# Optimization experiments

Hardware: AMD Instinct MI355X
Metric: run time of the kernel (lower is better)

Reference implementation:

```python
import jax, jax.numpy as jnp
import numpy as np

D_MODEL, D_K, D_V, H, N, B = 512, 64, 64, 8, 2048, 2


def _xavier(key, shape):
    fan_out, fan_in = shape
    a = jnp.sqrt(6.0 / (fan_in + fan_out))
    return jax.random.uniform(key, shape, jnp.float32, -a, a)


def setup_inputs() -> dict:
    key = jax.random.key(0)
    ks = jax.random.split(key, 12)
    inp = {
        "regions_out": jax.random.normal(ks[0], (B, N, D_MODEL), jnp.float32),
        "grids_out": jax.random.normal(ks[1], (B, N, D_MODEL), jnp.float32),
        "interests": jax.random.normal(ks[2], (B, N, D_MODEL), jnp.float32),
        "attention_mask_regions": jax.random.randint(ks[3], (B, 1, 1, N), 0, 2, jnp.int32),
        "attention_mask_grids": jax.random.randint(ks[4], (B, 1, 1, N), 0, 2, jnp.int32),
        "attention_weights": jax.random.uniform(ks[5], (B, 1, 1, N), jnp.float32),
        # nn.Linear params (weight [out,in], bias [out]); xavier_uniform weights, zero bias
        "Wq": _xavier(ks[6], (H * D_K, D_MODEL)), "bq": jnp.zeros((H * D_K,), jnp.float32),
        "Wk": _xavier(ks[7], (H * D_K, D_MODEL)), "bk": jnp.zeros((H * D_K,), jnp.float32),
        "Wv": _xavier(ks[8], (H * D_V, D_MODEL)), "bv": jnp.zeros((H * D_V,), jnp.float32),
        "Wq12": _xavier(ks[9], (H * D_K, D_MODEL)), "bq12": jnp.zeros((H * D_K,), jnp.float32),
        "Wo1": _xavier(ks[10], (D_MODEL, H * D_V)), "bo1": jnp.zeros((D_MODEL,), jnp.float32),
        "Wo2": _xavier(ks[11], (D_MODEL, H * D_V)), "bo2": jnp.zeros((D_MODEL,), jnp.float32),
    }
    return inp


def _proj(x, W, b, d):
    # x: [b, n, d_model] -> [b, h, n, d]
    b_s, n, _ = x.shape
    y = x @ W.T + b
    return y.reshape(b_s, n, H, d).transpose(0, 2, 1, 3)


def reference(regions_out, grids_out, interests, attention_mask_regions,
              attention_mask_grids, attention_weights,
              Wq, bq, Wk, bk, Wv, bv, Wq12, bq12, Wo1, bo1, Wo2, bo2):
    b_s, nq, _ = interests.shape
    scale = 1.0 / np.sqrt(D_K).astype(np.float32)

    q = _proj(interests, Wq, bq, D_K)          # [b,h,nq,dk]
    q1 = _proj(regions_out, Wq12, bq12, D_K)   # [b,h,nk1,dk]
    q2 = _proj(grids_out, Wq12, bq12, D_K)     # [b,h,nk1,dk]
    k1 = _proj(regions_out, Wk, bk, D_K)       # [b,h,nk1,dk]
    k2 = _proj(grids_out, Wk, bk, D_K)
    v1 = _proj(regions_out, Wv, bv, D_V)
    v2 = _proj(grids_out, Wv, bv, D_V)

    att1 = jnp.einsum("bhqd,bhkd->bhqk", q + q2, k1) * scale
    att2 = jnp.einsum("bhqd,bhkd->bhqk", q + q1, k2) * scale
    att1 = att1 * attention_weights
    att2 = att2 * attention_weights
    att1 = jnp.where(attention_mask_regions.astype(bool), -jnp.inf, att1)
    att2 = jnp.where(attention_mask_grids.astype(bool), -jnp.inf, att2)
    att1 = jax.nn.softmax(att1, axis=-1)
    att2 = jax.nn.softmax(att2, axis=-1)
    # dropout is identity in eval mode

    out1 = jnp.einsum("bhqk,bhkd->bhqd", att1, v1).transpose(0, 2, 1, 3).reshape(b_s, nq, H * D_V)
    out2 = jnp.einsum("bhqk,bhkd->bhqd", att2, v2).transpose(0, 2, 1, 3).reshape(b_s, nq, H * D_V)
    out1 = out1 @ Wo1.T + bo1
    out2 = out2 @ Wo2.T + bo2
    return (out1, out2)
```

## Files before the change

kernel.cpp:

```cpp
#include <hip/hip_runtime.h>
#include <hip/hip_bf16.h>

typedef __attribute__((ext_vector_type(8))) __bf16 bf16x8;
typedef __attribute__((ext_vector_type(4))) float f32x4;
typedef __attribute__((ext_vector_type(4))) int   i32x4;
typedef unsigned short u16;

#define WS_SEG 2097152

static __device__ __forceinline__ u16 f2b(float f) {
  __hip_bfloat16 h = __float2bfloat16(f);
  return __builtin_bit_cast(u16, h);
}
static __device__ __forceinline__ i32x4 cvt8(const float* __restrict__ p) {
  float4 a = *(const float4*)p;
  float4 b = *(const float4*)(p + 4);
  union { i32x4 v; u16 u[8]; } r;
  r.u[0]=f2b(a.x); r.u[1]=f2b(a.y); r.u[2]=f2b(a.z); r.u[3]=f2b(a.w);
  r.u[4]=f2b(b.x); r.u[5]=f2b(b.y); r.u[6]=f2b(b.z); r.u[7]=f2b(b.w);
  return r.v;
}
static __device__ __forceinline__ float fexp2(float x) {
  float r; asm("v_exp_f32 %0, %1" : "=v"(r) : "v"(x)); return r;
}
template<int C>
static __device__ __forceinline__ float dppf(float x) {
  int v = __builtin_amdgcn_update_dpp(__builtin_bit_cast(int, x),
                                      __builtin_bit_cast(int, x), C, 0xF, 0xF, false);
  return __builtin_bit_cast(float, v);
}
static __device__ __forceinline__ float rowsum16(float x) {
  x += dppf<0xB1>(x);
  x += dppf<0x4E>(x);
  x += dppf<0x141>(x);
  x += dppf<0x140>(x);
  return x;
}
static __device__ __forceinline__ void gld16(const u16* gp, u16* lp) {
  __builtin_amdgcn_global_load_lds(
      (const __attribute__((address_space(1))) void*)gp,
      (__attribute__((address_space(3))) void*)lp, 16, 0, 0);
}

__global__ __launch_bounds__(256) void convert_kernel(
    const float* __restrict__ regions, const float* __restrict__ grids,
    const float* __restrict__ interests,
    const float* __restrict__ Wq, const float* __restrict__ Wk,
    const float* __restrict__ Wv, const float* __restrict__ Wq12,
    const float* __restrict__ Wo1, const float* __restrict__ Wo2,
    u16* __restrict__ ws)
{
  const size_t i = (size_t)(blockIdx.x * 256 + threadIdx.x) * 8;
  const float* s; u16* d;
  if (i < 2097152)      { s = regions   + i;           d = ws + 6 * WS_SEG + i; }
  else if (i < 4194304) { s = grids     + (i - 2097152); d = ws + 7 * WS_SEG + (i - 2097152); }
  else if (i < 6291456) { s = interests + (i - 4194304); d = ws + 8 * WS_SEG + (i - 4194304); }
  else {
    const size_t j = i - 6291456;
    d = ws + 9 * WS_SEG + j;
    if (j < 262144)       s = Wq  + j;
    else if (j < 524288)  s = Wk  + (j - 262144);
    else if (j < 786432)  s = Wv  + (j - 524288);
    else if (j < 1048576) s = Wq12+ (j - 786432);
    else if (j < 1310720) s = Wo1 + (j - 1048576);
    else                  s = Wo2 + (j - 1310720);
  }
  *(i32x4*)d = cvt8(s);
}

template<int MT>
__global__ __launch_bounds__(256, 2) void gemm_all(
    const float* __restrict__ aw,
    const float* __restrict__ bq,  const float* __restrict__ bk,
    const float* __restrict__ bv,  const float* __restrict__ bq12,
    const float* __restrict__ bo1, const float* __restrict__ bo2,
    u16* __restrict__ ws, float* __restrict__ out, int phase)
{
  __shared__ u16 As[MT * 64];
  __shared__ u16 Bs[128 * 64];
  constexpr int MFR = MT / 32;

  const u16* regs_bf = ws + 6 * WS_SEG;
  const u16* grid_bf = ws + 7 * WS_SEG;
  const u16* intr_bf = ws + 8 * WS_SEG;
  const u16* Wt      = ws + 9 * WS_SEG;

  const u16 *A1 = nullptr, *A2 = nullptr, *B1 = nullptr, *B2 = nullptr;
  const float *bias1 = nullptr, *bias2 = nullptr;
  u16* dst16 = nullptr;
  float* dst32 = nullptr;
  int KT = 512, epi = 0;
  const int z = blockIdx.z;
  if (phase == 0) {
    if (z == 0)      { A1=intr_bf; A2=grid_bf; B1=Wt; B2=Wt+786432; KT=1024; bias1=bq; bias2=bq12; epi=0; dst16=ws+0*WS_SEG; }
    else if (z == 1) { A1=intr_bf; A2=regs_bf; B1=Wt; B2=Wt+786432; KT=1024; bias1=bq; bias2=bq12; epi=0; dst16=ws+1*WS_SEG; }
    else if (z == 2) { A1=regs_bf; B1=Wt+262144; bias1=bk; epi=1; dst16=ws+2*WS_SEG; }
    else if (z == 3) { A1=grid_bf; B1=Wt+262144; bias1=bk; epi=1; dst16=ws+3*WS_SEG; }
    else if (z == 4) { A1=regs_bf; B1=Wt+524288; bias1=bv; epi=3; dst16=ws+4*WS_SEG; }
    else             { A1=grid_bf; B1=Wt+524288; bias1=bv; epi=3; dst16=ws+5*WS_SEG; }
  } else {
    if (z == 0) { A1=ws+6*WS_SEG; B1=Wt+1048576; bias1=bo1; epi=2; dst32=out; }
    else        { A1=ws+7*WS_SEG; B1=Wt+1310720; bias1=bo2; epi=2; dst32=out + 2097152; }
  }
  const bool swp = (epi == 3);

  const int t = threadIdx.x;
  const int lane = t & 63, w = t >> 6;
  const int l15 = lane & 15, q4 = lane >> 4;
  const int m0 = blockIdx.y * MT, j0 = blockIdx.x * 128;
  const int ro = (w >> 1) * (MT / 2), co = (w & 1) * 64;

  f32x4 acc[MFR][4];
  for (int i = 0; i < MFR; i++)
    for (int j = 0; j < 4; j++) acc[i][j] = (f32x4){0.f, 0.f, 0.f, 0.f};

  for (int k0 = 0; k0 < KT; k0 += 64) {
    const u16* pa; const u16* pb; int kk = k0, ra, rb;
    if (swp)           { pa = B1; pb = A1; ra = j0; rb = m0; }
    else if (kk < 512) { pa = A1; pb = B1; ra = m0; rb = j0; }
    else               { pa = A2; pb = B2; ra = m0; rb = j0; kk -= 512; }
    __syncthreads();
#pragma unroll
    for (int c = 0; c < MFR; c++) {
      const int cidx = w * MFR + c;
      const int row = cidx * 8 + (lane >> 3);
      const int cg = (lane & 7) ^ (row & 7);
      gld16(&pa[(ra + row) * 512 + kk + cg * 8], &As[cidx * 512]);
    }
#pragma unroll
    for (int c = 0; c < 4; c++) {
      const int cidx = w * 4 + c;
      const int row = cidx * 8 + (lane >> 3);
      const int cg = (lane & 7) ^ (row & 7);
      gld16(&pb[(rb + row) * 512 + kk + cg * 8], &Bs[cidx * 512]);
    }
    __syncthreads();
#pragma unroll
    for (int h = 0; h < 2; h++) {
      bf16x8 af[MFR], bfr[4];
#pragma unroll
      for (int i = 0; i < MFR; i++) {
        const int r = ro + i * 16 + l15;
        af[i] = *(const bf16x8*)&As[r * 64 + (((h * 4 + q4) ^ (r & 7)) * 8)];
      }
#pragma unroll
      for (int i = 0; i < 4; i++) {
        const int r = co + i * 16 + l15;
        bfr[i] = *(const bf16x8*)&Bs[r * 64 + (((h * 4 + q4) ^ (r & 7)) * 8)];
      }
#pragma unroll
      for (int mt = 0; mt < MFR; mt++)
#pragma unroll
        for (int nt = 0; nt < 4; nt++)
          acc[mt][nt] = __builtin_amdgcn_mfma_f32_16x16x32_bf16(af[mt], bfr[nt], acc[mt][nt], 0, 0, 0);
    }
  }

#pragma unroll
  for (int nt = 0; nt < 4; nt++) {
    if (epi == 3) {
      const int token = m0 + co + nt * 16 + l15;
      const int bb = token >> 11, nn = token & 2047;
#pragma unroll
      for (int mt = 0; mt < MFR; mt++)
#pragma unroll
        for (int r = 0; r < 4; r++) {
          const int hd = j0 + ro + mt * 16 + q4 * 4 + r;
          dst16[(bb * 512 + hd) * 2048 + nn] = f2b(acc[mt][nt][r] + bias1[hd]);
        }
    } else {
      const int j = j0 + co + nt * 16 + l15;
      float bsum = bias1[j];
      if (bias2) bsum += bias2[j];
#pragma unroll
      for (int mt = 0; mt < MFR; mt++)
#pragma unroll
        for (int r = 0; r < 4; r++) {
          const int m = m0 + ro + mt * 16 + q4 * 4 + r;
          float v = acc[mt][nt][r] + bsum;
          if (epi == 2) {
            dst32[m * 512 + j] = v;
          } else {
            const int b = m >> 11, nn = m & 2047, h = j >> 6, d = j & 63;
            if (epi == 1) v *= 0.18033688f * aw[b * 2048 + nn];
            dst16[((b * 8 + h) * 2048 + nn) * 64 + d] = f2b(v);
          }
        }
    }
  }
}

__global__ __launch_bounds__(256, 2) void attn_kernel(
    const int* __restrict__ mask_r, const int* __restrict__ mask_g,
    u16* __restrict__ ws)
{
  const int qt = blockIdx.x, bh = blockIdx.y, path = blockIdx.z;
  const int b = bh >> 3, h = bh & 7;
  const u16* Q  = (path ? ws + 1 * WS_SEG : ws + 0 * WS_SEG) + bh * (2048 * 64);
  const u16* K  = (path ? ws + 3 * WS_SEG : ws + 2 * WS_SEG) + bh * (2048 * 64);
  const u16* Vg = (path ? ws + 5 * WS_SEG : ws + 4 * WS_SEG) + (b * 512 + h * 64) * 2048;
  const int* mask = (path ? mask_g : mask_r) + b * 2048;
  u16* O = (path ? ws + 7 * WS_SEG : ws + 6 * WS_SEG) + (b * 2048 + qt * 128) * 512 + h * 64;

  __shared__ u16 Ks[64 * 64];
  __shared__ u16 Vs[64 * 64];
  __shared__ u16 Ps[128 * 64];
  __shared__ float Ms[2048];

  const int t = threadIdx.x, lane = t & 63, w = t >> 6;
  const int l15 = lane & 15, q4 = lane >> 4;

  {
    const int4 a = *(const int4*)&mask[t * 8];
    const int4 c = *(const int4*)&mask[t * 8 + 4];
    float4 f1, f2v;
    f1.x = (a.x ? -1e30f : 0.f) - 16.f; f1.y = (a.y ? -1e30f : 0.f) - 16.f;
    f1.z = (a.z ? -1e30f : 0.f) - 16.f; f1.w = (a.w ? -1e30f : 0.f) - 16.f;
    f2v.x = (c.x ? -1e30f : 0.f) - 16.f; f2v.y = (c.y ? -1e30f : 0.f) - 16.f;
    f2v.z = (c.z ? -1e30f : 0.f) - 16.f; f2v.w = (c.w ? -1e30f : 0.f) - 16.f;
    *(float4*)&Ms[t * 8] = f1;
    *(float4*)&Ms[t * 8 + 4] = f2v;
  }

  bf16x8 qf[2][2];
#pragma unroll
  for (int mt = 0; mt < 2; mt++) {
    const int qrow = qt * 128 + w * 32 + mt * 16 + l15;
    qf[mt][0] = *(const bf16x8*)&Q[qrow * 64 + q4 * 8];
    qf[mt][1] = *(const bf16x8*)&Q[qrow * 64 + 32 + q4 * 8];
  }

  float l_run[2][4];
  f32x4 o_acc[2][4];
#pragma unroll
  for (int mt = 0; mt < 2; mt++) {
#pragma unroll
    for (int r = 0; r < 4; r++) l_run[mt][r] = 0.f;
#pragma unroll
    for (int d = 0; d < 4; d++) o_acc[mt][d] = (f32x4){0.f, 0.f, 0.f, 0.f};
  }

  for (int kt = 0; kt < 32; kt++) {
    __syncthreads();
#pragma unroll
    for (int c = 0; c < 2; c++) {
      const int cidx = w * 2 + c;
      const int row = cidx * 8 + (lane >> 3);
      const int cg = (lane & 7) ^ (row & 7);
      gld16(&K[(kt * 64 + row) * 64 + cg * 8], &Ks[cidx * 512]);
      gld16(&Vg[row * 2048 + kt * 64 + cg * 8], &Vs[cidx * 512]);
    }
    __syncthreads();

    f32x4 s[2][4];
#pragma unroll
    for (int mt = 0; mt < 2; mt++)
#pragma unroll
      for (int nt = 0; nt < 4; nt++) s[mt][nt] = (f32x4){0.f, 0.f, 0.f, 0.f};
#pragma unroll
    for (int nt = 0; nt < 4; nt++)
#pragma unroll
      for (int ss = 0; ss < 2; ss++) {
        const int r = nt * 16 + l15;
        bf16x8 kf = *(const bf16x8*)&Ks[r * 64 + (((ss * 4 + q4) ^ (r & 7)) * 8)];
        s[0][nt] = __builtin_amdgcn_mfma_f32_16x16x32_bf16(qf[0][ss], kf, s[0][nt], 0, 0, 0);
        s[1][nt] = __builtin_amdgcn_mfma_f32_16x16x32_bf16(qf[1][ss], kf, s[1][nt], 0, 0, 0);
      }

#pragma unroll
    for (int nt = 0; nt < 4; nt++) {
      const float bias = Ms[kt * 64 + nt * 16 + l15];
#pragma unroll
      for (int mt = 0; mt < 2; mt++)
#pragma unroll
        for (int r = 0; r < 4; r++) {
          const float p = fexp2(s[mt][nt][r] + bias);
          s[mt][nt][r] = p;
          l_run[mt][r] += p;
        }
    }

#pragma unroll
    for (int mt = 0; mt < 2; mt++)
#pragma unroll
      for (int nt = 0; nt < 4; nt++) {
        const int cg = 2 * nt + (l15 >> 3);
#pragma unroll
        for (int r = 0; r < 4; r++) {
          const int row = w * 32 + mt * 16 + q4 * 4 + r;
          Ps[row * 64 + ((cg ^ (row & 7)) * 8) + (l15 & 7)] = f2b(s[mt][nt][r]);
        }
      }
    asm volatile("s_waitcnt lgkmcnt(0)" ::: "memory");

#pragma unroll
    for (int ss = 0; ss < 2; ss++) {
      bf16x8 pf[2];
#pragma unroll
      for (int mt = 0; mt < 2; mt++) {
        const int row = w * 32 + mt * 16 + l15;
        const int cg = (4 * ss + q4) ^ (row & 7);
        pf[mt] = *(const bf16x8*)&Ps[row * 64 + cg * 8];
      }
#pragma unroll
      for (int dt = 0; dt < 4; dt++) {
        const int r = dt * 16 + l15;
        bf16x8 vf = *(const bf16x8*)&Vs[r * 64 + (((ss * 4 + q4) ^ (r & 7)) * 8)];
        o_acc[0][dt] = __builtin_amdgcn_mfma_f32_16x16x32_bf16(pf[0], vf, o_acc[0][dt], 0, 0, 0);
        o_acc[1][dt] = __builtin_amdgcn_mfma_f32_16x16x32_bf16(pf[1], vf, o_acc[1][dt], 0, 0, 0);
      }
    }
  }

#pragma unroll
  for (int mt = 0; mt < 2; mt++)
#pragma unroll
    for (int r = 0; r < 4; r++) {
      const float inv = 1.f / rowsum16(l_run[mt][r]);
#pragma unroll
      for (int dt = 0; dt < 4; dt++) {
        O[(w * 32 + mt * 16 + q4 * 4 + r) * 512 + dt * 16 + l15] = f2b(o_acc[mt][dt][r] * inv);
      }
    }
}

extern "C" void kernel_launch(void* const* d_in, const int* in_sizes, int n_in,
                              void* d_out, int out_size, void* d_ws, size_t ws_size,
                              hipStream_t stream) {
  const float* regions   = (const float*)d_in[0];
  const float* grids     = (const float*)d_in[1];
  const float* interests = (const float*)d_in[2];
  const int*   mask_r    = (const int*)d_in[3];
  const int*   mask_g    = (const int*)d_in[4];
  const float* aw        = (const float*)d_in[5];
  const float* Wq  = (const float*)d_in[6];  const float* bq  = (const float*)d_in[7];
  const float* Wk  = (const float*)d_in[8];  const float* bk  = (const float*)d_in[9];
  const float* Wv  = (const float*)d_in[10]; const float* bv  = (const float*)d_in[11];
  const float* Wq12= (const float*)d_in[12]; const float* bq12= (const float*)d_in[13];
  const float* Wo1 = (const float*)d_in[14]; const float* bo1 = (const float*)d_in[15];
  const float* Wo2 = (const float*)d_in[16]; const float* bo2 = (const float*)d_in[17];
  u16*   ws  = (u16*)d_ws;
  float* out = (float*)d_out;

  convert_kernel<<<3840, 256, 0, stream>>>(regions, grids, interests,
      Wq, Wk, Wv, Wq12, Wo1, Wo2, ws);
  gemm_all<128><<<dim3(4, 32, 6), 256, 0, stream>>>(aw, bq, bk, bv, bq12, bo1, bo2,
      ws, out, 0);
  attn_kernel<<<dim3(16, 16, 2), 256, 0, stream>>>(mask_r, mask_g, ws);
  gemm_all<64><<<dim3(4, 64, 2), 256, 0, stream>>>(aw, bq, bk, bv, bq12, bo1, bo2,
      ws, out, 1);
}
```

Baseline: 202.4 us.

## Stage GEMM and attention epilogues through LDS for coalesced 16-byte stores

The projection GEMM epilogue now writes bf16 results into swizzled shared memory and then issues coalesced 16-byte global stores instead of scattered 2-byte stores. The Q/K layout changes from head-major [b,h,n,64] to token-major [b,n,512], and the attention kernel's addressing is updated to match. The attention output is staged through Ps the same way before being stored. This aims to cut uncoalesced store traffic, at the cost of extra LDS round trips and syncs that rely on the per-wave LDS regions not overlapping.

Result: no change. 203.7 us (+0.6%).

```diff
diff --git a/kernel.cpp b/kernel.cpp
--- a/kernel.cpp
+++ b/kernel.cpp
@@ -156,36 +156,69 @@
     }
   }
 
-#pragma unroll
-  for (int nt = 0; nt < 4; nt++) {
-    if (epi == 3) {
-      const int token = m0 + co + nt * 16 + l15;
-      const int bb = token >> 11, nn = token & 2047;
-#pragma unroll
-      for (int mt = 0; mt < MFR; mt++)
-#pragma unroll
-        for (int r = 0; r < 4; r++) {
-          const int hd = j0 + ro + mt * 16 + q4 * 4 + r;
-          dst16[(bb * 512 + hd) * 2048 + nn] = f2b(acc[mt][nt][r] + bias1[hd]);
-        }
-    } else {
+  if (epi == 2) {
+#pragma unroll
+    for (int nt = 0; nt < 4; nt++) {
       const int j = j0 + co + nt * 16 + l15;
-      float bsum = bias1[j];
-      if (bias2) bsum += bias2[j];
+      const float bsum = bias1[j];
 #pragma unroll
       for (int mt = 0; mt < MFR; mt++)
 #pragma unroll
         for (int r = 0; r < 4; r++) {
           const int m = m0 + ro + mt * 16 + q4 * 4 + r;
-          float v = acc[mt][nt][r] + bsum;
-          if (epi == 2) {
-            dst32[m * 512 + j] = v;
-          } else {
-            const int b = m >> 11, nn = m & 2047, h = j >> 6, d = j & 63;
-            if (epi == 1) v *= 0.18033688f * aw[b * 2048 + nn];
-            dst16[((b * 8 + h) * 2048 + nn) * 64 + d] = f2b(v);
-          }
+          dst32[m * 512 + j] = acc[mt][nt][r] + bsum;
         }
+    }
+    return;
+  }
+
+  __syncthreads();
+  u16* Es = ((w < 2) ? As : Bs) + (w & 1) * 4096;
+
+  if (epi == 3) {
+#pragma unroll
+    for (int mt = 0; mt < MFR; mt++)
+#pragma unroll
+      for (int r = 0; r < 4; r++) {
+        const int rr = mt * 16 + q4 * 4 + r;
+        const float bias = bias1[j0 + ro + rr];
+#pragma unroll
+        for (int nt = 0; nt < 4; nt++)
+          Es[rr * 64 + (((nt * 2 + (l15 >> 3)) ^ (rr & 7)) * 8) + (l15 & 7)] =
+              f2b(acc[mt][nt][r] + bias);
+      }
+  } else {
+    float bsum4[4];
+#pragma unroll
+    for (int nt = 0; nt < 4; nt++) {
+      const int j = j0 + co + nt * 16 + l15;
+      bsum4[nt] = bias1[j] + (bias2 ? bias2[j] : 0.f);
+    }
+#pragma unroll
+    for (int mt = 0; mt < MFR; mt++)
+#pragma unroll
+      for (int r = 0; r < 4; r++) {
+        const int rr = mt * 16 + q4 * 4 + r;
+        const float awm = (epi == 1) ? 0.18033688f * aw[m0 + ro + rr] : 1.f;
+#pragma unroll
+        for (int nt = 0; nt < 4; nt++)
+          Es[rr * 64 + (((nt * 2 + (l15 >> 3)) ^ (rr & 7)) * 8) + (l15 & 7)] =
+              f2b((acc[mt][nt][r] + bsum4[nt]) * awm);
+      }
+  }
+  asm volatile("s_waitcnt lgkmcnt(0)" ::: "memory");
+
+#pragma unroll
+  for (int g = 0; g < 8; g++) {
+    const int rr2 = g * 8 + (lane >> 3);
+    i32x4 val = *(const i32x4*)&Es[rr2 * 64 + (((lane & 7) ^ (rr2 & 7)) * 8)];
+    if (epi == 3) {
+      const int hd = j0 + ro + rr2;
+      const int token0 = m0 + co;
+      *(i32x4*)&dst16[((size_t)(token0 >> 11) * 512 + hd) * 2048 + (token0 & 2047) + (lane & 7) * 8] = val;
+    } else {
+      const int tk = m0 + ro + rr2;
+      *(i32x4*)&dst16[(size_t)tk * 512 + j0 + co + (lane & 7) * 8] = val;
     }
   }
 }
@@ -196,11 +229,11 @@
 {
   const int qt = blockIdx.x, bh = blockIdx.y, path = blockIdx.z;
   const int b = bh >> 3, h = bh & 7;
-  const u16* Q  = (path ? ws + 1 * WS_SEG : ws + 0 * WS_SEG) + bh * (2048 * 64);
-  const u16* K  = (path ? ws + 3 * WS_SEG : ws + 2 * WS_SEG) + bh * (2048 * 64);
-  const u16* Vg = (path ? ws + 5 * WS_SEG : ws + 4 * WS_SEG) + (b * 512 + h * 64) * 2048;
+  const u16* Q  = (path ? ws + 1 * WS_SEG : ws + 0 * WS_SEG) + (size_t)(b * 2048 + qt * 128) * 512 + h * 64;
+  const u16* K  = (path ? ws + 3 * WS_SEG : ws + 2 * WS_SEG) + (size_t)(b * 2048) * 512 + h * 64;
+  const u16* Vg = (path ? ws + 5 * WS_SEG : ws + 4 * WS_SEG) + (size_t)(b * 512 + h * 64) * 2048;
   const int* mask = (path ? mask_g : mask_r) + b * 2048;
-  u16* O = (path ? ws + 7 * WS_SEG : ws + 6 * WS_SEG) + (b * 2048 + qt * 128) * 512 + h * 64;
+  u16* O = (path ? ws + 7 * WS_SEG : ws + 6 * WS_SEG) + (size_t)(b * 2048 + qt * 128) * 512 + h * 64;
 
   __shared__ u16 Ks[64 * 64];
   __shared__ u16 Vs[64 * 64];
@@ -225,9 +258,9 @@
   bf16x8 qf[2][2];
 #pragma unroll
   for (int mt = 0; mt < 2; mt++) {
-    const int qrow = qt * 128 + w * 32 + mt * 16 + l15;
-    qf[mt][0] = *(const bf16x8*)&Q[qrow * 64 + q4 * 8];
-    qf[mt][1] = *(const bf16x8*)&Q[qrow * 64 + 32 + q4 * 8];
+    const int qrow = w * 32 + mt * 16 + l15;
+    qf[mt][0] = *(const bf16x8*)&Q[qrow * 512 + q4 * 8];
+    qf[mt][1] = *(const bf16x8*)&Q[qrow * 512 + 32 + q4 * 8];
   }
 
   float l_run[2][4];
@@ -247,7 +280,7 @@
       const int cidx = w * 2 + c;
       const int row = cidx * 8 + (lane >> 3);
       const int cg = (lane & 7) ^ (row & 7);
-      gld16(&K[(kt * 64 + row) * 64 + cg * 8], &Ks[cidx * 512]);
+      gld16(&K[(size_t)(kt * 64 + row) * 512 + cg * 8], &Ks[cidx * 512]);
       gld16(&Vg[row * 2048 + kt * 64 + cg * 8], &Vs[cidx * 512]);
     }
     __syncthreads();
@@ -312,16 +345,29 @@
     }
   }
 
+  float inv[2][4];
 #pragma unroll
   for (int mt = 0; mt < 2; mt++)
 #pragma unroll
+    for (int r = 0; r < 4; r++) inv[mt][r] = 1.f / rowsum16(l_run[mt][r]);
+
+#pragma unroll
+  for (int mt = 0; mt < 2; mt++)
+#pragma unroll
     for (int r = 0; r < 4; r++) {
-      const float inv = 1.f / rowsum16(l_run[mt][r]);
-#pragma unroll
-      for (int dt = 0; dt < 4; dt++) {
-        O[(w * 32 + mt * 16 + q4 * 4 + r) * 512 + dt * 16 + l15] = f2b(o_acc[mt][dt][r] * inv);
-      }
-    }
+      const int row = w * 32 + mt * 16 + q4 * 4 + r;
+#pragma unroll
+      for (int dt = 0; dt < 4; dt++)
+        Ps[row * 64 + (((dt * 2 + (l15 >> 3)) ^ (row & 7)) * 8) + (l15 & 7)] =
+            f2b(o_acc[mt][dt][r] * inv[mt][r]);
+    }
+  asm volatile("s_waitcnt lgkmcnt(0)" ::: "memory");
+#pragma unroll
+  for (int g = 0; g < 4; g++) {
+    const int rl = w * 32 + g * 8 + (lane >> 3);
+    i32x4 val = *(const i32x4*)&Ps[rl * 64 + (((lane & 7) ^ (rl & 7)) * 8)];
+    *(i32x4*)&O[(size_t)rl * 512 + (lane & 7) * 8] = val;
+  }
 }
 
 extern "C" void kernel_launch(void* const* d_in, const int* in_sizes, int n_in,
```
